# Optimization experiments

Measured on AMD Instinct MI355X. Metric: run time of the kernel, lower is better.

## Reference

```python
import jax, jax.numpy as jnp
import numpy as np

B, T, H, W = 8, 10, 128, 128
WIDTH, NL = 64, 4
MT, MH, MW = 4, 8, 8
H_PRED = 5
MIN_STD = 1e-4


def setup_inputs() -> dict:
    key = jax.random.key(0)
    ks = jax.random.split(key, 12)
    scale = 1.0 / (WIDTH * WIDTH)
    return {
        "frames": jax.random.uniform(ks[0], (B, T, H, W), dtype=jnp.float32),
        "times": jax.random.uniform(ks[1], (B, T), dtype=jnp.float32),
        # lift: Conv3d(c_in=2 -> width, k=1)
        "lift_w": jax.random.normal(ks[2], (WIDTH, 2), dtype=jnp.float32) * 0.5,
        "lift_b": jnp.zeros((WIDTH,), jnp.float32),
        # spectral weights: (layer, quadrant, in, out, mt, mh, mw, re/im)
        "spec_w": jax.random.uniform(ks[3], (NL, 4, WIDTH, WIDTH, MT, MH, MW, 2), dtype=jnp.float32) * scale,
        # skip 1x1 Conv3d per layer
        "skip_w": jax.random.normal(ks[4], (NL, WIDTH, WIDTH), dtype=jnp.float32) * (1.0 / np.sqrt(WIDTH)),
        "skip_b": jnp.zeros((NL, WIDTH), jnp.float32),
        # temporal aggregation Conv3d kernel (h_ctx,1,1): (out, in, T)
        "agg_w": jax.random.normal(ks[5], (WIDTH, WIDTH, T), dtype=jnp.float32) * (1.0 / np.sqrt(WIDTH * T)),
        "agg_b": jnp.zeros((WIDTH,), jnp.float32),
        "fc1_w": jax.random.normal(ks[6], (WIDTH + 2, 128), dtype=jnp.float32) * (1.0 / np.sqrt(WIDTH + 2)),
        "fc1_b": jnp.zeros((128,), jnp.float32),
        "fc2_w": jax.random.normal(ks[7], (128, 2 * H_PRED), dtype=jnp.float32) * (1.0 / np.sqrt(128)),
        "fc2_b": jnp.zeros((2 * H_PRED,), jnp.float32),
    }


def _spectral_conv(x, wl):
    # x: (B, C, T, H, W); wl: (4, C, C, MT, MH, MW, 2) real/imag
    w = wl[..., 0] + 1j * wl[..., 1]  # (4, C, C, MT, MH, MW) complex
    x_ft = jnp.fft.rfftn(x, axes=(-3, -2, -1), norm="ortho")  # (B,C,T,H,W//2+1)
    Bc, C, Tt, Hh, Wf = x_ft.shape

    def mul(blk, wq):
        return jnp.einsum("bixyz,ioxyz->boxyz", blk, wq)

    out_ft = jnp.zeros((Bc, C, Tt, Hh, Wf), dtype=x_ft.dtype)
    out_ft = out_ft.at[:, :, :MT, :MH, :MW].set(mul(x_ft[:, :, :MT, :MH, :MW], w[0]))
    out_ft = out_ft.at[:, :, :MT, Hh - MH:, :MW].set(mul(x_ft[:, :, :MT, Hh - MH:, :MW], w[1]))
    out_ft = out_ft.at[:, :, Tt - MT:, :MH, :MW].set(mul(x_ft[:, :, Tt - MT:, :MH, :MW], w[2]))
    out_ft = out_ft.at[:, :, Tt - MT:, Hh - MH:, :MW].set(mul(x_ft[:, :, Tt - MT:, Hh - MH:, :MW], w[3]))
    return jnp.fft.irfftn(out_ft, s=(Tt, x.shape[-2], x.shape[-1]), axes=(-3, -2, -1), norm="ortho")


def reference(frames, times, lift_w, lift_b, spec_w, skip_w, skip_b,
              agg_w, agg_b, fc1_w, fc1_b, fc2_w, fc2_b):
    gelu = lambda v: jax.nn.gelu(v, approximate=False)
    # feature volume: (B, 2, T, H, W) = [frames, broadcast times]
    t_feat = jnp.broadcast_to(times[:, None, :, None, None], (B, 1, T, H, W))
    feat = jnp.concatenate([frames[:, None], t_feat], axis=1)
    # lift (1x1x1 conv)
    x = jnp.einsum("bcthw,oc->bothw", feat, lift_w) + lift_b[None, :, None, None, None]
    for l in range(NL):
        sx = _spectral_conv(x, spec_w[l])
        sk = jnp.einsum("bithw,oi->bothw", x, skip_w[l]) + skip_b[l][None, :, None, None, None]
        x = gelu(sx + sk)
    # temporal aggregation: valid conv over full T -> (B, C, H, W)
    x = jnp.einsum("bithw,oit->bohw", x, agg_w) + agg_b[None, :, None, None]
    # (x, y) grid channels
    gx = jnp.broadcast_to(jnp.linspace(-1.0, 1.0, W)[None, :], (H, W))
    gy = jnp.broadcast_to(jnp.linspace(-1.0, 1.0, H)[:, None], (H, W))
    grid = jnp.broadcast_to(jnp.stack([gx, gy], 0)[None], (B, 2, H, W))
    x = jnp.concatenate([x, grid], axis=1)  # (B, C+2, H, W)
    x = jnp.transpose(x, (0, 2, 3, 1))      # (B, H, W, C+2)
    x = gelu(x @ fc1_w + fc1_b)
    out = x @ fc2_w + fc2_b                 # (B, H, W, 2*h_pred)
    mu = out[..., 0::2]
    sigma = jax.nn.softplus(out[..., 1::2]) + MIN_STD
    return jnp.concatenate([mu, sigma], axis=-1)  # (B, H, W, 2*h_pred)
```

## Files before the change

kernel.cpp:

```cpp
#include <hip/hip_runtime.h>
#include <math.h>


#define TWO_PI 6.2831853071795864769f
#define ORTHO_SC 2.4705294220065465e-3f

typedef unsigned short u16;
typedef _Float16 f16;
typedef __attribute__((ext_vector_type(8))) _Float16 f16x8;
typedef __attribute__((ext_vector_type(4))) float f32x4;

#define MFMAH(acc, a, b) acc = __builtin_amdgcn_mfma_f32_16x16x32_f16(a, b, acc, 0, 0, 0)

__device__ __forceinline__ u16 f16b(float v) {
  f16 h = (f16)v;
  return __builtin_bit_cast(u16, h);
}
__device__ __forceinline__ float f16lo(float v) {
  f16 h = (f16)v;
  return v - (float)h;
}
__device__ __forceinline__ float f16f(u16 b) {
  return (float)__builtin_bit_cast(f16, b);
}
__device__ __forceinline__ float gelu_fast(float x) {
  float u = 0.7978845608f * (x + 0.044715f * x * x * x);
  float a = fminf(u * 2.885390082f, 30.0f);
  float e = __builtin_exp2f(a);
  return x * e * __builtin_amdgcn_rcpf(e + 1.0f);
}

__global__ __launch_bounds__(256) void k_prep2(const float* __restrict__ skip_w,
                                               const float* __restrict__ agg_w,
                                               const float* __restrict__ fc1_w,
                                               const float* __restrict__ fc1_b,
                                               u16* __restrict__ swf,
                                               u16* __restrict__ awf,
                                               u16* __restrict__ Tt,
                                               float2* __restrict__ twf,
                                               u16* __restrict__ Ef,
                                               u16* __restrict__ f1f) {
  int e = blockIdx.x*256 + threadIdx.x;
  if (e < 32768) {
    int j = e & 7, lane = (e >> 3) & 63, half = (e >> 9) & 1, ks = (e >> 10) & 1;
    int strip = (e >> 11) & 3, layer = e >> 13;
    int co = strip*16 + (lane & 15);
    int ci = ks*32 + (lane >> 4)*8 + j;
    float v = skip_w[((size_t)(layer*64) + co)*64 + ci];
    swf[e] = half ? f16b(f16lo(v)) : f16b(v);
  } else if (e < 114688) {
    int ee = e - 32768;
    int j = ee & 7, lane = (ee >> 3) & 63;
    int v9 = ee >> 9;
    int half = v9 & 1; v9 >>= 1;
    int ks = v9 & 1; v9 >>= 1;
    int t = v9 % 10, strip = v9 / 10;
    int co = strip*16 + (lane & 15);
    int ci = ks*32 + (lane >> 4)*8 + j;
    float v = agg_w[((size_t)co*64 + ci)*10 + t];
    awf[ee] = half ? f16b(f16lo(v)) : f16b(v);
  } else if (e < 122880) {
    int ee = e - 114688;
    int half = ee >> 12, r = ee & 4095, w = r >> 5, kk = r & 31;
    int m = kk >> 1;
    float val;
    if (kk >= 16) val = 0.f;
    else if (kk == 0) val = 1.f;
    else if (kk == 1) val = 0.f;
    else {
      float th = TWO_PI * (float)m * (float)w / 128.0f;
      val = (kk & 1) ? (-2.f*sinf(th)) : (2.f*cosf(th));
    }
    Tt[ee] = half ? f16b(f16lo(val)) : f16b(val);
  } else if (e < 123904) {
    int ee = e - 122880;
    int w = ee >> 3, k = ee & 7;
    float th = TWO_PI * (float)k * (float)w / 128.0f;
    twf[ee] = make_float2(cosf(th), -sinf(th));
  } else if (e < 125952) {
    int ee = e - 123904;
    int j = ee & 7, lane = (ee >> 3) & 63, kc = ee >> 9;
    int n = lane & 15, g = lane >> 4;
    int w = kc*32 + g*8 + j;
    int k = n >> 1;
    float th = TWO_PI * (float)k * (float)w / 128.0f;
    float val = (n & 1) ? (-sinf(th)) : cosf(th);
    Ef[ee] = f16b(val);
    Ef[2048 + ee] = f16b(f16lo(val));
  } else if (e < 150528) {
    int ee = e - 125952;
    int j = ee & 7, lane = (ee >> 3) & 63, hl = (ee >> 9) & 1;
    int rest = ee >> 10;
    int kc = rest % 3, strip = rest / 3;
    int o = strip*16 + (lane & 15);
    int k = kc*32 + (lane >> 4)*8 + j;
    float v;
    if (k < 66) v = fc1_w[(size_t)k*128 + o];
    else if (k == 66) v = fc1_b[o];
    else v = 0.f;
    f1f[ee] = hl ? f16b(f16lo(v)) : f16b(v);
  }
}

__global__ __launch_bounds__(128) void k_lift_fwdW(const float* __restrict__ frames,
                                                   const float* __restrict__ times,
                                                   const float* __restrict__ lift_w,
                                                   const float* __restrict__ lift_b,
                                                   const float2* __restrict__ twf,
                                                   u16* __restrict__ xT,
                                                   u16* __restrict__ xw16) {
  __shared__ u16 xs[64][130];
  __shared__ float2 tws[128][8];
  __shared__ float fr[128];
  __shared__ float lw0[64], lw1a[64];
  int bth = blockIdx.x;
  int h = bth & 127; int bt = bth >> 7; int t = bt % 10, b = bt / 10;
  int tid = threadIdx.x;
  for (int i = tid; i < 1024; i += 128) tws[i >> 3][i & 7] = twf[i];
  float tv = times[b*10 + t];
  fr[tid] = frames[((size_t)(b*10 + t)*128 + h)*128 + tid];
  if (tid < 64) { lw0[tid] = lift_w[2*tid]; lw1a[tid] = lift_w[2*tid+1]*tv + lift_b[tid]; }
  __syncthreads();
  {
    int w = tid;
    float f = fr[w];
    unsigned pk[32];
    #pragma unroll
    for (int q = 0; q < 32; ++q) {
      float v0 = f*lw0[2*q] + lw1a[2*q];
      float v1 = f*lw0[2*q+1] + lw1a[2*q+1];
      u16 h0 = f16b(v0), h1 = f16b(v1);
      xs[2*q][w] = h0; xs[2*q+1][w] = h1;
      pk[q] = (unsigned)h0 | ((unsigned)h1 << 16);
    }
    uint4* d4 = (uint4*)(xT + (size_t)bth*8192 + w*64);
    #pragma unroll
    for (int q = 0; q < 8; ++q)
      d4[q] = make_uint4(pk[4*q], pk[4*q+1], pk[4*q+2], pk[4*q+3]);
  }
  __syncthreads();
  {
    int lane = tid & 63, wv = tid >> 6;
    float ar[4] = {0,0,0,0}, ai[4] = {0,0,0,0};
    for (int w2 = 0; w2 < 128; ++w2) {
      float xu = f16f(xs[lane][w2]);
      #pragma unroll
      for (int kk = 0; kk < 4; ++kk) {
        float2 ew = tws[w2][wv*4 + kk];
        ar[kk] += xu*ew.x; ai[kk] += xu*ew.y;
      }
    }
    size_t row = ((size_t)(b*64 + lane)*10 + t)*128 + h;
    unsigned p0 = (unsigned)f16b(ar[0]) | ((unsigned)f16b(ai[0]) << 16);
    unsigned p1 = (unsigned)f16b(ar[1]) | ((unsigned)f16b(ai[1]) << 16);
    unsigned p2 = (unsigned)f16b(ar[2]) | ((unsigned)f16b(ai[2]) << 16);
    unsigned p3 = (unsigned)f16b(ar[3]) | ((unsigned)f16b(ai[3]) << 16);
    *(uint4*)(xw16 + row*16 + wv*8) = make_uint4(p0, p1, p2, p3);
  }
}

__global__ __launch_bounds__(256) void k_fwdHT(const unsigned* __restrict__ xw32,
                                               float2* __restrict__ xf) {
  __shared__ unsigned tile[2][1024];
  __shared__ float2 parts1[1024];
  __shared__ float2 tw128[128];
  int bc = blockIdx.x;
  int b = bc >> 6, c = bc & 63;
  int tid = threadIdx.x;
  if (tid < 128) {
    float s, co; sincosf(TWO_PI * (float)tid / 128.0f, &s, &co);
    tw128[tid] = make_float2(co, -s);
  }
  int tpar = tid >> 7, j = tid & 127;
  int khi = j >> 3, kwi = j & 7;
  int kh = (khi < 8) ? khi : (112 + khi);
  float accr[8], acci[8];
  #pragma unroll
  for (int k = 0; k < 8; ++k) { accr[k] = 0.f; acci[k] = 0.f; }
  for (int tt = 0; tt < 5; ++tt) {
    __syncthreads();
    for (int u = tid; u < 2048; u += 256) {
      int tg = u >> 10, idx = u & 1023;
      tile[tg][idx] = xw32[((size_t)bc*10 + tg*5 + tt)*1024 + idx];
    }
    __syncthreads();
    float xr = 0.f, xi = 0.f;
    for (int h = 0; h < 128; ++h) {
      unsigned uv = tile[tpar][h*8 + kwi];
      float vx = f16f((u16)uv);
      float vy = f16f((u16)(uv >> 16));
      float2 tw = tw128[(h*kh) & 127];
      xr += vx*tw.x - vy*tw.y;
      xi += vx*tw.y + vy*tw.x;
    }
    int t = tpar*5 + tt;
    float sb, cb; sincosf(TWO_PI * (float)t / 10.0f, &sb, &cb);
    float p_r[10], p_i[10];
    p_r[0] = 1.f; p_i[0] = 0.f; p_r[1] = cb; p_i[1] = -sb;
    #pragma unroll
    for (int k = 2; k < 10; ++k) {
      p_r[k] = p_r[k-1]*p_r[1] - p_i[k-1]*p_i[1];
      p_i[k] = p_r[k-1]*p_i[1] + p_i[k-1]*p_r[1];
    }
    #pragma unroll
    for (int kti = 0; kti < 8; ++kti) {
      int kt = (kti < 4) ? kti : kti + 2;
      accr[kti] += xr*p_r[kt] - xi*p_i[kt];
      acci[kti] += xr*p_i[kt] + xi*p_r[kt];
    }
  }
  __syncthreads();
  if (tpar == 1) {
    #pragma unroll
    for (int kti = 0; kti < 8; ++kti)
      parts1[j*8 + kti] = make_float2(accr[kti], acci[kti]);
  }
  __syncthreads();
  if (tpar == 0) {
    #pragma unroll
    for (int kti = 0; kti < 8; ++kti) {
      float2 bq = parts1[j*8 + kti];
      xf[((size_t)b*1024 + kti*128 + j)*64 + c] =
          make_float2((accr[kti] + bq.x)*ORTHO_SC, (acci[kti] + bq.y)*ORTHO_SC);
    }
  }
}

__global__ __launch_bounds__(256) void k_mix(const float2* __restrict__ xf,
                                             const float* __restrict__ spec_w_l,
                                             float2* __restrict__ yf) {
  __shared__ float2 xfs[8][4][64];
  int m0 = blockIdx.x * 4;
  for (int i = threadIdx.x; i < 2048; i += 256) {
    int bb = i >> 8, mi = (i >> 6) & 3, ci = i & 63;
    xfs[bb][mi][ci] = xf[((size_t)bb*1024 + m0 + mi)*64 + ci];
  }
  __syncthreads();
  int co = threadIdx.x & 63, mi = threadIdx.x >> 6;
  int m = m0 + mi;
  int kti = m >> 7, khi = (m >> 3) & 15, kwi = m & 7;
  int q = ((kti >= 4) ? 2 : 0) + ((khi >= 8) ? 1 : 0);
  int modeidx = ((kti & 3)*8 + (khi & 7))*8 + kwi;
  const float2* wp = (const float2*)spec_w_l
                     + ((size_t)(q*64)*64 + co)*256 + modeidx;
  float accr[8], acci[8];
  #pragma unroll
  for (int bb = 0; bb < 8; ++bb) { accr[bb] = 0.f; acci[bb] = 0.f; }
  for (int ci = 0; ci < 64; ++ci) {
    float2 wv = wp[(size_t)ci*16384];
    #pragma unroll
    for (int bb = 0; bb < 8; ++bb) {
      float2 xv = xfs[bb][mi][ci];
      accr[bb] += xv.x*wv.x - xv.y*wv.y;
      acci[bb] += xv.x*wv.y + xv.y*wv.x;
    }
  }
  #pragma unroll
  for (int bb = 0; bb < 8; ++bb)
    yf[((size_t)bb*64 + co)*1024 + m] = make_float2(accr[bb], acci[bb]);
}

__global__ __launch_bounds__(256) void k_invTH(const float2* __restrict__ yf,
                                               unsigned* __restrict__ zh16) {
  __shared__ float2 ybuf[1024];
  __shared__ float2 ztb[2][128];
  __shared__ float2 tw128[128];
  int bc = blockIdx.x;
  int b = bc >> 6, c = bc & 63;
  int tid = threadIdx.x;
  for (int u = tid; u < 1024; u += 256) ybuf[u] = yf[(size_t)bc*1024 + u];
  if (tid < 128) {
    float s, co; sincosf(TWO_PI * (float)tid / 128.0f, &s, &co);
    tw128[tid] = make_float2(co, s);
  }
  int tpar = tid >> 7, j = tid & 127;
  __syncthreads();
  for (int tt = 0; tt < 5; ++tt) {
    int t = tt*2 + tpar;
    {
      float sb, cb; sincosf(TWO_PI * (float)t / 10.0f, &sb, &cb);
      float p_r[10], p_i[10];
      p_r[0] = 1.f; p_i[0] = 0.f; p_r[1] = cb; p_i[1] = sb;
      #pragma unroll
      for (int k = 2; k < 10; ++k) {
        p_r[k] = p_r[k-1]*p_r[1] - p_i[k-1]*p_i[1];
        p_i[k] = p_r[k-1]*p_i[1] + p_i[k-1]*p_r[1];
      }
      float zr = 0.f, zi = 0.f;
      #pragma unroll
      for (int kti = 0; kti < 8; ++kti) {
        int kt = (kti < 4) ? kti : kti + 2;
        float2 v = ybuf[kti*128 + j];
        zr += v.x*p_r[kt] - v.y*p_i[kt];
        zi += v.x*p_i[kt] + v.y*p_r[kt];
      }
      ztb[tpar][j] = make_float2(zr*ORTHO_SC, zi*ORTHO_SC);
    }
    __syncthreads();
    {
      int h = j;
      float ar[8], ai[8];
      #pragma unroll
      for (int kw = 0; kw < 8; ++kw) { ar[kw] = 0.f; ai[kw] = 0.f; }
      #pragma unroll
      for (int khi = 0; khi < 16; ++khi) {
        int kh = (khi < 8) ? khi : (112 + khi);
        float2 tw = tw128[(h*kh) & 127];
        #pragma unroll
        for (int kw = 0; kw < 8; ++kw) {
          float2 v = ztb[tpar][khi*8 + kw];
          ar[kw] += v.x*tw.x - v.y*tw.y;
          ai[kw] += v.x*tw.y + v.y*tw.x;
        }
      }
      unsigned* dst = zh16 + (((size_t)(b*10 + t)*128 + h)*64 + c)*8;
      #pragma unroll
      for (int kw = 0; kw < 8; ++kw)
        dst[kw] = (unsigned)f16b(ar[kw]) | ((unsigned)f16b(ai[kw]) << 16);
    }
    __syncthreads();
  }
}

__global__ __launch_bounds__(256, 4) void k_invW_mfma(const u16* __restrict__ xTin,
                                                      const unsigned* __restrict__ zh16,
                                                      const u16* __restrict__ swf_l,
                                                      const u16* __restrict__ Tt,
                                                      const u16* __restrict__ Ef,
                                                      const float* __restrict__ skb,
                                                      u16* __restrict__ xTo,
                                                      u16* __restrict__ xw16,
                                                      int do_dft) {
  __shared__ __align__(16) char smem[20480];
  u16* B = (u16*)smem;
  u16* zAh = (u16*)(smem + 18432);
  int tid = threadIdx.x;
  int bth = blockIdx.x;
  int lane = tid & 63;
  int wq = tid >> 6;
  int cL = lane & 15;
  int g = lane >> 4;

  f16x8 Th[2];
  #pragma unroll
  for (int t2 = 0; t2 < 2; ++t2) {
    int wrow = wq*32 + t2*16 + cL;
    Th[t2] = *(const f16x8*)(Tt + wrow*32 + g*8);
  }
  {
    const uint4* xsrc = (const uint4*)(xTin + (size_t)bth*8192);
    for (int u = tid; u < 1024; u += 256) {
      int w = u >> 3, c = u & 7;
      ((uint4*)(B + w*72))[c] = xsrc[u];
    }
  }
  {
    const unsigned* zsrc = zh16 + (size_t)bth*512;
    for (int u = tid; u < 512; u += 256) {
      int co = u >> 3, m = u & 7;
      *(unsigned*)(zAh + co*16 + 2*m) = zsrc[u];
    }
  }
  __syncthreads();

  f32x4 acc[4][2];
  #pragma unroll
  for (int s = 0; s < 4; ++s)
    #pragma unroll
    for (int t2 = 0; t2 < 2; ++t2) acc[s][t2] = (f32x4){0.f,0.f,0.f,0.f};

  #pragma unroll
  for (int kb = 0; kb < 2; ++kb) {
    f16x8 Ah[4], Al[4];
    #pragma unroll
    for (int s = 0; s < 4; ++s) {
      Ah[s] = *(const f16x8*)(swf_l + (size_t)(s*2048 + kb*1024 + lane*8));
      Al[s] = *(const f16x8*)(swf_l + (size_t)(s*2048 + kb*1024 + 512 + lane*8));
    }
    #pragma unroll
    for (int t2 = 0; t2 < 2; ++t2) {
      int wrow = wq*32 + t2*16 + cL;
      f16x8 bh = *(const f16x8*)(B + wrow*72 + kb*32 + g*8);
      #pragma unroll
      for (int s = 0; s < 4; ++s) {
        MFMAH(acc[s][t2], Ah[s], bh);
        MFMAH(acc[s][t2], Al[s], bh);
      }
    }
  }
  {
    f16x8 Azh[4];
    f16x8 zero8 = {0,0,0,0,0,0,0,0};
    #pragma unroll
    for (int s = 0; s < 4; ++s)
      Azh[s] = (g < 2) ? *(const f16x8*)(zAh + (s*16 + cL)*16 + g*8) : zero8;
    #pragma unroll
    for (int t2 = 0; t2 < 2; ++t2) {
      #pragma unroll
      for (int s = 0; s < 4; ++s) {
        MFMAH(acc[s][t2], Azh[s], Th[t2]);
      }
    }
  }

  __syncthreads();
  unsigned* out32 = (unsigned*)smem;
  #pragma unroll
  for (int s = 0; s < 4; ++s) {
    float4 b4 = *(const float4*)(skb + s*16 + g*4);
    float bb[4] = {b4.x, b4.y, b4.z, b4.w};
    #pragma unroll
    for (int t2 = 0; t2 < 2; ++t2) {
      int w = wq*32 + t2*16 + cL;
      u16 gb[4];
      #pragma unroll
      for (int r = 0; r < 4; ++r) {
        float val = acc[s][t2][r] + bb[r];
        gb[r] = f16b(gelu_fast(val));
      }
      out32[(s*8 + g*2 + 0)*130 + w] = (unsigned)gb[0] | ((unsigned)gb[1] << 16);
      out32[(s*8 + g*2 + 1)*130 + w] = (unsigned)gb[2] | ((unsigned)gb[3] << 16);
    }
  }
  __syncthreads();
  {
    uint4* xdst = (uint4*)(xTo + (size_t)bth*8192);
    for (int u = tid; u < 1024; u += 256) {
      int w = u >> 3, c = u & 7;
      unsigned r0 = out32[(c*4 + 0)*130 + w];
      unsigned r1 = out32[(c*4 + 1)*130 + w];
      unsigned r2 = out32[(c*4 + 2)*130 + w];
      unsigned r3 = out32[(c*4 + 3)*130 + w];
      xdst[u] = make_uint4(r0, r1, r2, r3);
    }
  }
  if (do_dft) {
    f32x4 acc2 = (f32x4){0.f,0.f,0.f,0.f};
    int row = wq*8 + (cL >> 1);
    int sh = (cL & 1) * 16;
    #pragma unroll
    for (int kc = 0; kc < 4; ++kc) {
      const unsigned* p = out32 + row*130 + kc*32 + g*8;
      uint2 d0 = *(const uint2*)(p);
      uint2 d1 = *(const uint2*)(p + 2);
      uint2 d2 = *(const uint2*)(p + 4);
      uint2 d3 = *(const uint2*)(p + 6);
      f16x8 a;
      a[0] = __builtin_bit_cast(f16, (u16)(d0.x >> sh));
      a[1] = __builtin_bit_cast(f16, (u16)(d0.y >> sh));
      a[2] = __builtin_bit_cast(f16, (u16)(d1.x >> sh));
      a[3] = __builtin_bit_cast(f16, (u16)(d1.y >> sh));
      a[4] = __builtin_bit_cast(f16, (u16)(d2.x >> sh));
      a[5] = __builtin_bit_cast(f16, (u16)(d2.y >> sh));
      a[6] = __builtin_bit_cast(f16, (u16)(d3.x >> sh));
      a[7] = __builtin_bit_cast(f16, (u16)(d3.y >> sh));
      f16x8 eh = *(const f16x8*)(Ef + (kc*64 + lane)*8);
      f16x8 el = *(const f16x8*)(Ef + 2048 + (kc*64 + lane)*8);
      MFMAH(acc2, a, eh);
      MFMAH(acc2, a, el);
    }
    int h = bth & 127; int bt = bth >> 7; int t = bt % 10, b = bt / 10;
    #pragma unroll
    for (int r = 0; r < 4; ++r) {
      int co = wq*16 + g*4 + r;
      size_t row2 = ((size_t)(b*64 + co)*10 + t)*128 + h;
      xw16[row2*16 + cL] = f16b(acc2[r]);
    }
  }
}

__global__ __launch_bounds__(256) void k_agg_mfma(const u16* __restrict__ xT,
                                                  const u16* __restrict__ awf,
                                                  const float* __restrict__ agg_b,
                                                  float* __restrict__ xa) {
  __shared__ __align__(16) u16 B[128*72];
  int tid = threadIdx.x;
  int bid = blockIdx.x;
  int h = bid & 127, b = bid >> 7;
  int lane = tid & 63;
  int wq = tid >> 6;
  int cL = lane & 15;
  int g = lane >> 4;

  f32x4 acc[4][2];
  #pragma unroll
  for (int s = 0; s < 4; ++s)
    #pragma unroll
    for (int t2 = 0; t2 < 2; ++t2) acc[s][t2] = (f32x4){0.f,0.f,0.f,0.f};

  for (int t = 0; t < 10; ++t) {
    __syncthreads();
    {
      const uint4* xsrc = (const uint4*)(xT + ((size_t)(b*10 + t)*128 + h)*8192);
      for (int u = tid; u < 1024; u += 256) {
        int w = u >> 3, c = u & 7;
        ((uint4*)(B + w*72))[c] = xsrc[u];
      }
    }
    __syncthreads();
    #pragma unroll
    for (int kc = 0; kc < 2; ++kc) {
      f16x8 Ah[4], Al[4];
      #pragma unroll
      for (int s = 0; s < 4; ++s) {
        const u16* af = awf + (size_t)((s*10 + t)*4 + kc*2)*512;
        Ah[s] = *(const f16x8*)(af + lane*8);
        Al[s] = *(const f16x8*)(af + 512 + lane*8);
      }
      #pragma unroll
      for (int t2 = 0; t2 < 2; ++t2) {
        int wrow = wq*32 + t2*16 + cL;
        f16x8 bh = *(const f16x8*)(B + wrow*72 + kc*32 + g*8);
        #pragma unroll
        for (int s = 0; s < 4; ++s) {
          MFMAH(acc[s][t2], Ah[s], bh);
          MFMAH(acc[s][t2], Al[s], bh);
        }
      }
    }
  }

  #pragma unroll
  for (int s = 0; s < 4; ++s) {
    float4 b4 = *(const float4*)(agg_b + s*16 + g*4);
    float bb[4] = {b4.x, b4.y, b4.z, b4.w};
    #pragma unroll
    for (int t2 = 0; t2 < 2; ++t2) {
      int w = wq*32 + t2*16 + cL;
      #pragma unroll
      for (int r = 0; r < 4; ++r) {
        int co = s*16 + g*4 + r;
        xa[((size_t)(b*64 + co)*128 + h)*128 + w] = acc[s][t2][r] + bb[r];
      }
    }
  }
}

__global__ __launch_bounds__(256) void k_head_mfma(const float* __restrict__ xa,
                                                   const u16* __restrict__ f1f,
                                                   const float* __restrict__ fc2_w,
                                                   const float* __restrict__ fc2_b,
                                                   float* __restrict__ out) {
  __shared__ __align__(16) u16 B[128*128];
  __shared__ float w2s[1280];
  int tid = threadIdx.x;
  int bid = blockIdx.x;
  int h = bid & 127, b = bid >> 7;
  for (int i = tid; i < 1280; i += 256) w2s[i] = fc2_w[i];
  for (int u = tid; u < 2048; u += 256) {
    int co = u >> 5, w4 = u & 31;
    float4 v = *(const float4*)(xa + ((size_t)(b*64 + co)*128 + h)*128 + w4*4);
    float vv[4] = {v.x, v.y, v.z, v.w};
    int kg = co >> 3, kj = co & 7;
    #pragma unroll
    for (int jj = 0; jj < 4; ++jj) {
      int w = w4*4 + jj;
      B[w*128 + ((kg ^ (w & 7)) << 3) + kj] = f16b(vv[jj]);
    }
  }
  for (int u = tid; u < 512; u += 256) {
    int w = u & 127, kgo = u >> 7;
    int kg = 8 + kgo;
    u16* dst = &B[w*128 + ((kg ^ (w & 7)) << 3)];
    if (kgo == 0) {
      float gx = -1.f + 2.f*(float)w/127.f;
      float gy = -1.f + 2.f*(float)h/127.f;
      dst[0] = f16b(gx); dst[1] = f16b(gy); dst[2] = f16b(1.f);
      dst[3] = 0; dst[4] = 0; dst[5] = 0; dst[6] = 0; dst[7] = 0;
    } else {
      #pragma unroll
      for (int q = 0; q < 8; ++q) dst[q] = 0;
    }
  }
  __syncthreads();

  int lane = tid & 63, wq = tid >> 6, cL = lane & 15, g = lane >> 4;
  f32x4 acc[8][2];
  #pragma unroll
  for (int s = 0; s < 8; ++s)
    #pragma unroll
    for (int t2 = 0; t2 < 2; ++t2) acc[s][t2] = (f32x4){0.f,0.f,0.f,0.f};

  #pragma unroll
  for (int kc = 0; kc < 3; ++kc) {
    f16x8 bfr[2];
    #pragma unroll
    for (int t2 = 0; t2 < 2; ++t2) {
      int wrow = wq*32 + t2*16 + cL;
      int kg = kc*4 + g;
      bfr[t2] = *(const f16x8*)(&B[wrow*128 + ((kg ^ (wrow & 7)) << 3)]);
    }
    #pragma unroll
    for (int s = 0; s < 8; ++s) {
      f16x8 Ah = *(const f16x8*)(f1f + (size_t)(((s*3 + kc)*2 + 0)*64 + lane)*8);
      f16x8 Al = *(const f16x8*)(f1f + (size_t)(((s*3 + kc)*2 + 1)*64 + lane)*8);
      #pragma unroll
      for (int t2 = 0; t2 < 2; ++t2) {
        MFMAH(acc[s][t2], Ah, bfr[t2]);
        MFMAH(acc[s][t2], Al, bfr[t2]);
      }
    }
  }

  float o2[2][10];
  #pragma unroll
  for (int t2 = 0; t2 < 2; ++t2)
    #pragma unroll
    for (int j = 0; j < 10; ++j) o2[t2][j] = 0.f;
  #pragma unroll
  for (int s = 0; s < 8; ++s) {
    #pragma unroll
    for (int t2 = 0; t2 < 2; ++t2) {
      #pragma unroll
      for (int r = 0; r < 4; ++r) {
        int o = s*16 + g*4 + r;
        float gl = gelu_fast(acc[s][t2][r]);
        #pragma unroll
        for (int j = 0; j < 10; ++j) o2[t2][j] += gl * w2s[o*10 + j];
      }
    }
  }
  #pragma unroll
  for (int t2 = 0; t2 < 2; ++t2)
    #pragma unroll
    for (int j = 0; j < 10; ++j) {
      float v = o2[t2][j];
      v += __shfl_xor(v, 16, 64);
      v += __shfl_xor(v, 32, 64);
      o2[t2][j] = v;
    }
  if (g == 0) {
    #pragma unroll
    for (int t2 = 0; t2 < 2; ++t2) {
      int w = wq*32 + t2*16 + cL;
      float* dst = out + ((size_t)bid*128 + w)*10;
      float tot[10];
      #pragma unroll
      for (int j = 0; j < 10; ++j) tot[j] = o2[t2][j] + fc2_b[j];
      #pragma unroll
      for (int k = 0; k < 5; ++k) dst[k] = tot[2*k];
      #pragma unroll
      for (int k = 0; k < 5; ++k) {
        float sv = tot[2*k+1];
        float sp = fmaxf(sv, 0.f) + log1pf(expf(-fabsf(sv)));
        dst[5 + k] = sp + 1e-4f;
      }
    }
  }
}

extern "C" void kernel_launch(void* const* d_in, const int* in_sizes, int n_in,
                              void* d_out, int out_size, void* d_ws, size_t ws_size,
                              hipStream_t stream) {
  const float* frames = (const float*)d_in[0];
  const float* times  = (const float*)d_in[1];
  const float* lift_w = (const float*)d_in[2];
  const float* lift_b = (const float*)d_in[3];
  const float* spec_w = (const float*)d_in[4];
  const float* skip_w = (const float*)d_in[5];
  const float* skip_b = (const float*)d_in[6];
  const float* agg_w  = (const float*)d_in[7];
  const float* agg_b  = (const float*)d_in[8];
  const float* fc1_w  = (const float*)d_in[9];
  const float* fc1_b  = (const float*)d_in[10];
  const float* fc2_w  = (const float*)d_in[11];
  const float* fc2_b  = (const float*)d_in[12];
  float* out = (float*)d_out;
  char* ws = (char*)d_ws;

  size_t off = 0;
  u16*      xT  = (u16*)(ws + off);      off += (size_t)10240*8192*2;
  u16*      xw16= (u16*)(ws + off);      off += (size_t)655360*16*2;
  float2*   xf  = (float2*)(ws + off);   off += (size_t)8*1024*64*8;
  float2*   yf  = (float2*)(ws + off);   off += (size_t)8*1024*64*8;
  unsigned* zh16= (unsigned*)(ws + off); off += (size_t)10240*512*4;
  float*    xa  = (float*)(ws + off);    off += (size_t)8*64*128*128*4;
  u16*      swf = (u16*)(ws + off);      off += (size_t)32768*2;
  u16*      awf = (u16*)(ws + off);      off += (size_t)81920*2;
  u16*      Tt  = (u16*)(ws + off);      off += (size_t)8192*2;
  float2*   twf = (float2*)(ws + off);   off += (size_t)1024*8;
  u16*      Ef  = (u16*)(ws + off);      off += (size_t)4096*2;
  u16*      f1f = (u16*)(ws + off);      off += (size_t)24576*2;

  k_prep2<<<588, 256, 0, stream>>>(skip_w, agg_w, fc1_w, fc1_b,
                                   swf, awf, Tt, twf, Ef, f1f);
  k_lift_fwdW<<<10240, 128, 0, stream>>>(frames, times, lift_w, lift_b, twf, xT, xw16);

  for (int l = 0; l < 4; ++l) {
    k_fwdHT<<<512, 256, 0, stream>>>((const unsigned*)xw16, xf);
    k_mix<<<256, 256, 0, stream>>>(xf, spec_w + (size_t)l*4*64*64*256*2, yf);
    k_invTH<<<512, 256, 0, stream>>>(yf, zh16);
    k_invW_mfma<<<10240, 256, 0, stream>>>(xT, zh16, swf + (size_t)l*8192, Tt, Ef,
                                           skip_b + l*64, xT, xw16, (l < 3) ? 1 : 0);
  }
  k_agg_mfma<<<1024, 256, 0, stream>>>(xT, awf, agg_b, xa);
  k_head_mfma<<<1024, 256, 0, stream>>>(xa, f1f, fc2_w, fc2_b, out);
}
```

Baseline: 937.9 us.

## Split k_mix across batch halves, store agg output as fp16, defer T-basis load

k_mix now handles 2 modes per block with each thread covering 4 batches, doubling the grid to 512 blocks for more parallelism but reloading spectral weights twice. The aggregation output buffer is stored as fp16 instead of fp32, halving its write and read traffic between the agg and head kernels. The head kernel had already converted these values to fp16, so the only added rounding is on the agg-plus-bias sum. The Tt fragment load in k_invW_mfma is moved next to its use to shorten register live ranges.

```diff
diff --git a/kernel.cpp b/kernel.cpp
--- a/kernel.cpp
+++ b/kernel.cpp
@@ -229,35 +229,35 @@
 __global__ __launch_bounds__(256) void k_mix(const float2* __restrict__ xf,
                                              const float* __restrict__ spec_w_l,
                                              float2* __restrict__ yf) {
-  __shared__ float2 xfs[8][4][64];
-  int m0 = blockIdx.x * 4;
-  for (int i = threadIdx.x; i < 2048; i += 256) {
-    int bb = i >> 8, mi = (i >> 6) & 3, ci = i & 63;
+  __shared__ float2 xfs[8][2][64];
+  int m0 = blockIdx.x * 2;
+  for (int i = threadIdx.x; i < 1024; i += 256) {
+    int bb = i >> 7, mi = (i >> 6) & 1, ci = i & 63;
     xfs[bb][mi][ci] = xf[((size_t)bb*1024 + m0 + mi)*64 + ci];
   }
   __syncthreads();
-  int co = threadIdx.x & 63, mi = threadIdx.x >> 6;
+  int co = threadIdx.x & 63, mi = (threadIdx.x >> 6) & 1, bh = threadIdx.x >> 7;
   int m = m0 + mi;
   int kti = m >> 7, khi = (m >> 3) & 15, kwi = m & 7;
   int q = ((kti >= 4) ? 2 : 0) + ((khi >= 8) ? 1 : 0);
   int modeidx = ((kti & 3)*8 + (khi & 7))*8 + kwi;
   const float2* wp = (const float2*)spec_w_l
                      + ((size_t)(q*64)*64 + co)*256 + modeidx;
-  float accr[8], acci[8];
-  #pragma unroll
-  for (int bb = 0; bb < 8; ++bb) { accr[bb] = 0.f; acci[bb] = 0.f; }
+  float accr[4], acci[4];
+  #pragma unroll
+  for (int bb = 0; bb < 4; ++bb) { accr[bb] = 0.f; acci[bb] = 0.f; }
   for (int ci = 0; ci < 64; ++ci) {
     float2 wv = wp[(size_t)ci*16384];
     #pragma unroll
-    for (int bb = 0; bb < 8; ++bb) {
-      float2 xv = xfs[bb][mi][ci];
+    for (int bb = 0; bb < 4; ++bb) {
+      float2 xv = xfs[bh*4 + bb][mi][ci];
       accr[bb] += xv.x*wv.x - xv.y*wv.y;
       acci[bb] += xv.x*wv.y + xv.y*wv.x;
     }
   }
   #pragma unroll
-  for (int bb = 0; bb < 8; ++bb)
-    yf[((size_t)bb*64 + co)*1024 + m] = make_float2(accr[bb], acci[bb]);
+  for (int bb = 0; bb < 4; ++bb)
+    yf[((size_t)(bh*4 + bb)*64 + co)*1024 + m] = make_float2(accr[bb], acci[bb]);
 }
 
 __global__ __launch_bounds__(256) void k_invTH(const float2* __restrict__ yf,
@@ -341,12 +341,6 @@
   int cL = lane & 15;
   int g = lane >> 4;
 
-  f16x8 Th[2];
-  #pragma unroll
-  for (int t2 = 0; t2 < 2; ++t2) {
-    int wrow = wq*32 + t2*16 + cL;
-    Th[t2] = *(const f16x8*)(Tt + wrow*32 + g*8);
-  }
   {
     const uint4* xsrc = (const uint4*)(xTin + (size_t)bth*8192);
     for (int u = tid; u < 1024; u += 256) {
@@ -396,9 +390,11 @@
       Azh[s] = (g < 2) ? *(const f16x8*)(zAh + (s*16 + cL)*16 + g*8) : zero8;
     #pragma unroll
     for (int t2 = 0; t2 < 2; ++t2) {
+      int wrow = wq*32 + t2*16 + cL;
+      f16x8 th = *(const f16x8*)(Tt + wrow*32 + g*8);
       #pragma unroll
       for (int s = 0; s < 4; ++s) {
-        MFMAH(acc[s][t2], Azh[s], Th[t2]);
+        MFMAH(acc[s][t2], Azh[s], th);
       }
     }
   }
@@ -472,7 +468,7 @@
 __global__ __launch_bounds__(256) void k_agg_mfma(const u16* __restrict__ xT,
                                                   const u16* __restrict__ awf,
                                                   const float* __restrict__ agg_b,
-                                                  float* __restrict__ xa) {
+                                                  u16* __restrict__ xa16) {
   __shared__ __align__(16) u16 B[128*72];
   int tid = threadIdx.x;
   int bid = blockIdx.x;
@@ -530,13 +526,13 @@
       #pragma unroll
       for (int r = 0; r < 4; ++r) {
         int co = s*16 + g*4 + r;
-        xa[((size_t)(b*64 + co)*128 + h)*128 + w] = acc[s][t2][r] + bb[r];
-      }
-    }
-  }
-}
-
-__global__ __launch_bounds__(256) void k_head_mfma(const float* __restrict__ xa,
+        xa16[((size_t)(b*64 + co)*128 + h)*128 + w] = f16b(acc[s][t2][r] + bb[r]);
+      }
+    }
+  }
+}
+
+__global__ __launch_bounds__(256) void k_head_mfma(const u16* __restrict__ xa16,
                                                    const u16* __restrict__ f1f,
                                                    const float* __restrict__ fc2_w,
                                                    const float* __restrict__ fc2_b,
@@ -549,13 +545,13 @@
   for (int i = tid; i < 1280; i += 256) w2s[i] = fc2_w[i];
   for (int u = tid; u < 2048; u += 256) {
     int co = u >> 5, w4 = u & 31;
-    float4 v = *(const float4*)(xa + ((size_t)(b*64 + co)*128 + h)*128 + w4*4);
-    float vv[4] = {v.x, v.y, v.z, v.w};
+    uint2 d = *(const uint2*)(xa16 + ((size_t)(b*64 + co)*128 + h)*128 + w4*4);
+    u16 vv[4] = {(u16)d.x, (u16)(d.x >> 16), (u16)d.y, (u16)(d.y >> 16)};
     int kg = co >> 3, kj = co & 7;
     #pragma unroll
     for (int jj = 0; jj < 4; ++jj) {
       int w = w4*4 + jj;
-      B[w*128 + ((kg ^ (w & 7)) << 3) + kj] = f16b(vv[jj]);
+      B[w*128 + ((kg ^ (w & 7)) << 3) + kj] = vv[jj];
     }
   }
   for (int u = tid; u < 512; u += 256) {
@@ -674,7 +670,7 @@
   float2*   xf  = (float2*)(ws + off);   off += (size_t)8*1024*64*8;
   float2*   yf  = (float2*)(ws + off);   off += (size_t)8*1024*64*8;
   unsigned* zh16= (unsigned*)(ws + off); off += (size_t)10240*512*4;
-  float*    xa  = (float*)(ws + off);    off += (size_t)8*64*128*128*4;
+  u16*      xa16= (u16*)(ws + off);      off += (size_t)8*64*128*128*2;
   u16*      swf = (u16*)(ws + off);      off += (size_t)32768*2;
   u16*      awf = (u16*)(ws + off);      off += (size_t)81920*2;
   u16*      Tt  = (u16*)(ws + off);      off += (size_t)8192*2;
@@ -688,11 +684,11 @@
 
   for (int l = 0; l < 4; ++l) {
     k_fwdHT<<<512, 256, 0, stream>>>((const unsigned*)xw16, xf);
-    k_mix<<<256, 256, 0, stream>>>(xf, spec_w + (size_t)l*4*64*64*256*2, yf);
+    k_mix<<<512, 256, 0, stream>>>(xf, spec_w + (size_t)l*4*64*64*256*2, yf);
     k_invTH<<<512, 256, 0, stream>>>(yf, zh16);
     k_invW_mfma<<<10240, 256, 0, stream>>>(xT, zh16, swf + (size_t)l*8192, Tt, Ef,
                                            skip_b + l*64, xT, xw16, (l < 3) ? 1 : 0);
   }
-  k_agg_mfma<<<1024, 256, 0, stream>>>(xT, awf, agg_b, xa);
-  k_head_mfma<<<1024, 256, 0, stream>>>(xa, f1f, fc2_w, fc2_b, out);
-}
+  k_agg_mfma<<<1024, 256, 0, stream>>>(xT, awf, agg_b, xa16);
+  k_head_mfma<<<1024, 256, 0, stream>>>(xa16, f1f, fc2_w, fc2_b, out);
+}
```

After: 1.024 ms. 9.2% more time.
